# Performance work log

Hardware: AMD Instinct MI355X
Metric: run time of the kernel (lower is better)

The kernel has to match this reference:

```python
import jax, jax.numpy as jnp
import numpy as np

B, N, D, H, K = 8, 1024, 1024, 64, 20


def setup_inputs() -> dict:
    key = jax.random.key(0)
    ks = jax.random.split(key, 8)
    s = 0.05
    return {
        "f1": jax.random.normal(ks[0], (B, N, D), jnp.float32),
        "f2": jax.random.normal(ks[1], (B, N, D), jnp.float32),
        "W1a": jax.random.normal(ks[2], (D, H), jnp.float32) * s,
        "b1a": jnp.zeros((H,), jnp.float32),
        "W2a": jax.random.normal(ks[3], (H, H), jnp.float32) * s,
        "b2a": jnp.zeros((H,), jnp.float32),
        "W1b": jax.random.normal(ks[4], (H, H), jnp.float32) * s,
        "b1b": jnp.zeros((H,), jnp.float32),
        "W2b": jax.random.normal(ks[5], (H, H), jnp.float32) * s,
        "b2b": jnp.zeros((H,), jnp.float32),
        "k": K,
    }


def _knn_idx(f, k):
    # f: [N, D] -> indices [N, k] of k nearest neighbors (self excluded)
    sq = jnp.sum(f * f, axis=-1)                      # [N]
    d = sq[:, None] + sq[None, :] - 2.0 * (f @ f.T)   # [N, N] squared dists
    n = f.shape[0]
    d = d + jnp.eye(n, dtype=f.dtype) * jnp.float32(1e10)  # exclude self-loop
    _, idx = jax.lax.top_k(-d, k)                     # smallest distances
    return idx


def _gin_layer(x, idx, W1, b1, W2, b2):
    # GINConv with eps=0: MLP(x + sum_{j in N(i)} x_j)
    agg = jnp.sum(x[idx], axis=1)                     # [N, D] neighbor-sum
    h = x + agg
    h = jnp.maximum(h @ W1 + b1, 0.0) @ W2 + b2
    return h


def reference(f1, f2, W1a, b1a, W2a, b2a, W1b, b1b, W2b, b2b, k):
    def encode(f):
        idx = _knn_idx(f, k)
        h = _gin_layer(f, idx, W1a, b1a, W2a, b2a)
        h = _gin_layer(h, idx, W1b, b1b, W2b, b2b)
        return h

    def per_sample(a, b):
        z1 = encode(a)                                # [N, H]
        z2 = encode(b)                                # [N, H]
        sim = z1 @ z2.T                               # [N, N]
        return jax.nn.softmax(sim, axis=1)

    return jax.vmap(per_sample)(f1, f2)               # [B, N, N]
```

## Files before the change

kernel.cpp:

```cpp
#include <hip/hip_runtime.h>
#include <hip/hip_bf16.h>
#include <math.h>

#define BATCH 8
#define NPTS  1024
#define DIM   1024
#define HID   64
#define KNN   20
#define NMAT  16
#define KPACK 3072

typedef __attribute__((ext_vector_type(8))) short short8;
typedef __attribute__((ext_vector_type(4))) float floatx4;

__device__ __forceinline__ const float* mat_base(const float* f1, const float* f2, int m) {
    return (m < BATCH) ? (f1 + (size_t)m * NPTS * DIM)
                       : (f2 + (size_t)(m - BATCH) * NPTS * DIM);
}

__device__ __forceinline__ unsigned short f2bf_bits(float v) {
    __hip_bfloat16 h = __float2bfloat16(v);
    return *(unsigned short*)&h;
}
__device__ __forceinline__ float bfbits2f(unsigned short b) {
    union { unsigned u; float f; } c; c.u = ((unsigned)b) << 16; return c.f;
}

__global__ __launch_bounds__(256) void split_ymlp_kernel(const float* __restrict__ f1,
                                                         const float* __restrict__ f2,
                                                         const float* __restrict__ W,
                                                         unsigned short* __restrict__ H,
                                                         float* __restrict__ sq,
                                                         float* __restrict__ y) {
    int row0 = blockIdx.x * 64;
    int m = row0 >> 10;
    const float* A = mat_base(f1, f2, m) + (size_t)(row0 & (NPTS - 1)) * DIM;
    unsigned short* Hb = H + (size_t)row0 * KPACK;
    __shared__ float As[64][20];
    __shared__ float Ws[16][HID];
    int tid = threadIdx.x;
    int r = tid >> 2, cq = (tid & 3) * 4;
    int ty = tid >> 4, tx = tid & 15;
    float acc[4][4];
    #pragma unroll
    for (int i = 0; i < 4; ++i)
        #pragma unroll
        for (int j = 0; j < 4; ++j) acc[i][j] = 0.f;
    float sqp = 0.f;
    unsigned short* Hr = Hb + (size_t)r * KPACK + cq;

    for (int kk = 0; kk < DIM; kk += 16) {
        float4 a = *(const float4*)&A[(size_t)r * DIM + kk + cq];
        {
            float vv[4] = {a.x, a.y, a.z, a.w};
            unsigned short h1[4], h2[4], h3[4];
            #pragma unroll
            for (int c = 0; c < 4; ++c) {
                unsigned short b1 = f2bf_bits(vv[c]);
                float r1 = vv[c] - bfbits2f(b1);
                unsigned short b2 = f2bf_bits(r1);
                float r2 = r1 - bfbits2f(b2);
                unsigned short b3 = f2bf_bits(r2);
                h1[c] = b1; h2[c] = b2; h3[c] = b3;
            }
            *(ushort4*)&Hr[kk]        = *(ushort4*)&h1[0];
            *(ushort4*)&Hr[1024 + kk] = *(ushort4*)&h2[0];
            *(ushort4*)&Hr[2048 + kk] = *(ushort4*)&h3[0];
            sqp += a.x * a.x + a.y * a.y + a.z * a.z + a.w * a.w;
        }
        *(float4*)&As[r][cq] = a;
        {
            int d = tid >> 4, hh = (tid & 15) * 4;
            *(float4*)&Ws[d][hh] = *(const float4*)&W[(size_t)(kk + d) * HID + hh];
        }
        __syncthreads();
        #pragma unroll
        for (int k = 0; k < 16; ++k) {
            float av[4];
            #pragma unroll
            for (int ii = 0; ii < 4; ++ii) av[ii] = As[ty * 4 + ii][k];
            float4 w = *(const float4*)&Ws[k][tx * 4];
            #pragma unroll
            for (int ii = 0; ii < 4; ++ii) {
                acc[ii][0] += av[ii] * w.x;
                acc[ii][1] += av[ii] * w.y;
                acc[ii][2] += av[ii] * w.z;
                acc[ii][3] += av[ii] * w.w;
            }
        }
        __syncthreads();
    }
    sqp += __shfl_down(sqp, 1);
    sqp += __shfl_down(sqp, 2);
    if ((tid & 3) == 0) sq[row0 + r] = sqp;
    #pragma unroll
    for (int ii = 0; ii < 4; ++ii)
        *(float4*)&y[(size_t)(row0 + ty * 4 + ii) * HID + tx * 4] = *(float4*)&acc[ii][0];
}

#define GRAM_STEP(CURAF, NXTAF, CBUF, NBUF, KN, ISSUE, WAITOP)                             \
  {                                                                                        \
    if (ISSUE) {                                                                           \
      _Pragma("unroll")                                                                    \
      for (int s = 0; s < 3; ++s)                                                          \
        _Pragma("unroll")                                                                  \
        for (int a = 0; a < 2; ++a)                                                        \
          NXTAF[s][a] = *(const short8*)&Hm[(size_t)(ti + ((w << 1) + a) * 16 + r16) * KPACK \
                                            + (size_t)(s << 10) + (KN) + (kc << 3)];       \
      _Pragma("unroll")                                                                    \
      for (int c = 0; c < 6; ++c) {                                                        \
        int ca = w * 6 + c; int seg = ca >> 3; int rb = ca & 7;                            \
        const unsigned short* gb = Hm + (size_t)(tj + rb * 16 + r16) * KPACK               \
                                      + (size_t)(seg << 10) + (KN) + (kc << 3);            \
        __builtin_amdgcn_global_load_lds(                                                  \
            (const __attribute__((address_space(1))) void*)gb,                             \
            (__attribute__((address_space(3))) void*)&Bsl[NBUF][ca * 512], 16, 0, 0);      \
      }                                                                                    \
    }                                                                                      \
    asm volatile(WAITOP ::: "memory");                                                     \
    __builtin_amdgcn_s_barrier();                                                          \
    asm volatile("" ::: "memory");                                                         \
    __builtin_amdgcn_s_setprio(1);                                                         \
    _Pragma("unroll")                                                                      \
    for (int sb = 0; sb < 3; ++sb) {                                                       \
      short8 bf[8];                                                                        \
      _Pragma("unroll")                                                                    \
      for (int b = 0; b < 8; ++b)                                                          \
        bf[b] = *(const short8*)&Bsl[CBUF][(sb * 8 + b) * 512 + lane * 8];                 \
      _Pragma("unroll")                                                                    \
      for (int sa = 0; sa < 3; ++sa) {                                                     \
        if (sa + sb > 2) continue;                                                         \
        _Pragma("unroll")                                                                  \
        for (int a = 0; a < 2; ++a)                                                        \
          _Pragma("unroll")                                                                \
          for (int b = 0; b < 8; ++b)                                                      \
            acc[a][b] = __builtin_amdgcn_mfma_f32_16x16x32_bf16(CURAF[sa][a], bf[b],       \
                                                                acc[a][b], 0, 0, 0);       \
      }                                                                                    \
    }                                                                                      \
    __builtin_amdgcn_s_setprio(0);                                                         \
    asm volatile("" ::: "memory");                                                         \
    __builtin_amdgcn_s_barrier();                                                          \
  }

__global__ __launch_bounds__(256, 2) void gram_mfma_kernel(const unsigned short* __restrict__ H,
                                                           const float* __restrict__ sq,
                                                           float* __restrict__ dist) {
    int bid = blockIdx.x;
    int xcd = bid & 7;
    int g = bid >> 3;
    int m = xcd + 8 * (g & 1);
    int t = g >> 1;
    int bi = 0;
    { int a = t; while (a >= 8 - bi) { a -= 8 - bi; ++bi; } t = a; }
    int bj = bi + t;
    int ti = bi << 7, tj = bj << 7;

    const unsigned short* Hm = H + (size_t)m * NPTS * KPACK;

    __shared__ __align__(16) unsigned short Bsl[3][24 * 512];

    int tid = threadIdx.x;
    int w = tid >> 6, lane = tid & 63;
    int r16 = lane & 15, kc = lane >> 4;

    floatx4 acc[2][8];
    #pragma unroll
    for (int a = 0; a < 2; ++a)
        #pragma unroll
        for (int b = 0; b < 8; ++b) acc[a][b] = (floatx4)0.f;

    short8 afA[3][2], afB[3][2], afC[3][2];

    #pragma unroll
    for (int s = 0; s < 3; ++s)
        #pragma unroll
        for (int a = 0; a < 2; ++a) {
            size_t rowb = (size_t)(ti + ((w << 1) + a) * 16 + r16) * KPACK + (size_t)(s << 10) + (kc << 3);
            afA[s][a] = *(const short8*)&Hm[rowb];
            afB[s][a] = *(const short8*)&Hm[rowb + 32];
        }
    #pragma unroll
    for (int c = 0; c < 6; ++c) {
        int ca = w * 6 + c; int seg = ca >> 3; int rb = ca & 7;
        const unsigned short* gb = Hm + (size_t)(tj + rb * 16 + r16) * KPACK
                                      + (size_t)(seg << 10) + (kc << 3);
        __builtin_amdgcn_global_load_lds(
            (const __attribute__((address_space(1))) void*)gb,
            (__attribute__((address_space(3))) void*)&Bsl[0][ca * 512], 16, 0, 0);
        __builtin_amdgcn_global_load_lds(
            (const __attribute__((address_space(1))) void*)(gb + 32),
            (__attribute__((address_space(3))) void*)&Bsl[1][ca * 512], 16, 0, 0);
    }

    #pragma unroll 1
    for (int t2 = 0; t2 < 30; t2 += 3) {
        GRAM_STEP(afA, afC, 0, 2, (t2 + 2) * 32, 1, "s_waitcnt vmcnt(24)");
        GRAM_STEP(afB, afA, 1, 0, (t2 + 3) * 32, 1, "s_waitcnt vmcnt(24)");
        GRAM_STEP(afC, afB, 2, 1, (t2 + 4) * 32, 1, "s_waitcnt vmcnt(24)");
    }
    GRAM_STEP(afA, afC, 0, 2, 0, 0, "s_waitcnt vmcnt(12)");
    GRAM_STEP(afB, afC, 1, 2, 0, 0, "s_waitcnt vmcnt(0)");

    const float* sqm = sq + m * NPTS;
    #pragma unroll
    for (int a = 0; a < 2; ++a) {
        int i0 = ti + ((w << 1) + a) * 16 + (lane >> 4) * 4;
        #pragma unroll
        for (int b = 0; b < 8; ++b) {
            int j = tj + b * 16 + (lane & 15);
            float sqj = sqm[j];
            #pragma unroll
            for (int r = 0; r < 4; ++r) {
                int i = i0 + r;
                float v = sqm[i] + sqj - 2.f * acc[a][b][r];
                if (i == j) v += 1e10f;
                dist[((size_t)m * NPTS + i) * NPTS + j] = v;
                if (bi != bj) dist[((size_t)m * NPTS + j) * NPTS + i] = v;
            }
        }
    }
}

__global__ __launch_bounds__(256) void topk_kernel(const float* __restrict__ dist,
                                                   int* __restrict__ knn_idx) {
    int tid = threadIdx.x;
    int wave = tid >> 6, lane = tid & 63;
    int row = blockIdx.x * 4 + wave;
    const float* d = dist + (size_t)row * NPTS;
    float v[16];
    #pragma unroll
    for (int s = 0; s < 16; ++s) v[s] = d[s * 64 + lane];
    int myj = 0;
    for (int sel = 0; sel < KNN; ++sel) {
        float bv = v[0]; int bs = 0;
        #pragma unroll
        for (int s = 1; s < 16; ++s)
            if (v[s] < bv) { bv = v[s]; bs = s; }
        int bj = bs * 64 + lane;
        #pragma unroll
        for (int off = 1; off < 64; off <<= 1) {
            float ov = __shfl_xor(bv, off);
            int   oj = __shfl_xor(bj, off);
            if (ov < bv || (ov == bv && oj < bj)) { bv = ov; bj = oj; }
        }
        if ((bj & 63) == lane) v[bj >> 6] = 3e38f;
        if (lane == sel) myj = bj;
    }
    if (lane < KNN) knn_idx[(size_t)row * KNN + lane] = myj;
}

__global__ __launch_bounds__(256) void t1h1_kernel(const float* __restrict__ y,
                                                   const int* __restrict__ knn_idx,
                                                   const float* __restrict__ W,
                                                   const float* __restrict__ bias1,
                                                   const float* __restrict__ bias2,
                                                   float* __restrict__ h1) {
    int row0 = blockIdx.x * 64;
    int m = row0 >> 10;
    __shared__ int nb[64 * KNN];
    __shared__ float t1s[64][65];
    __shared__ float Ws[64][HID];
    __shared__ float b1s[HID], b2s[HID];
    int tid = threadIdx.x;
    for (int k = tid; k < 64 * KNN; k += 256) nb[k] = knn_idx[(size_t)row0 * KNN + k];
    for (int k = tid; k < 64 * HID; k += 256) Ws[k >> 6][k & 63] = W[k];
    if (tid < HID) { b1s[tid] = bias1[tid]; b2s[tid] = bias2[tid]; }
    __syncthreads();
    {
        int r = tid >> 2, c0 = (tid & 3) * 16;
        const float* yr = y + (size_t)(row0 + r) * HID + c0;
        float4 a[4];
        #pragma unroll
        for (int q = 0; q < 4; ++q) a[q] = *(const float4*)&yr[q * 4];
        const float* ym = y + (size_t)(m << 10) * HID;
        #pragma unroll
        for (int t = 0; t < KNN; ++t) {
            const float* yn = ym + (size_t)nb[r * KNN + t] * HID + c0;
            #pragma unroll
            for (int q = 0; q < 4; ++q) {
                float4 v = *(const float4*)&yn[q * 4];
                a[q].x += v.x; a[q].y += v.y; a[q].z += v.z; a[q].w += v.w;
            }
        }
        #pragma unroll
        for (int q = 0; q < 4; ++q) {
            int c = c0 + q * 4;
            t1s[r][c + 0] = fmaxf(a[q].x + b1s[c + 0], 0.f);
            t1s[r][c + 1] = fmaxf(a[q].y + b1s[c + 1], 0.f);
            t1s[r][c + 2] = fmaxf(a[q].z + b1s[c + 2], 0.f);
            t1s[r][c + 3] = fmaxf(a[q].w + b1s[c + 3], 0.f);
        }
    }
    __syncthreads();
    int ty = tid >> 4, tx = tid & 15;
    float acc[4][4];
    #pragma unroll
    for (int i = 0; i < 4; ++i)
        #pragma unroll
        for (int j = 0; j < 4; ++j) acc[i][j] = 0.f;
    #pragma unroll
    for (int k = 0; k < HID; ++k) {
        float a[4];
        #pragma unroll
        for (int ii = 0; ii < 4; ++ii) a[ii] = t1s[ty * 4 + ii][k];
        float4 w = *(const float4*)&Ws[k][tx * 4];
        #pragma unroll
        for (int ii = 0; ii < 4; ++ii) {
            acc[ii][0] += a[ii] * w.x;
            acc[ii][1] += a[ii] * w.y;
            acc[ii][2] += a[ii] * w.z;
            acc[ii][3] += a[ii] * w.w;
        }
    }
    #pragma unroll
    for (int ii = 0; ii < 4; ++ii) {
        float o[4];
        #pragma unroll
        for (int jj = 0; jj < 4; ++jj) o[jj] = acc[ii][jj] + b2s[tx * 4 + jj];
        *(float4*)&h1[(size_t)(row0 + ty * 4 + ii) * HID + tx * 4] = *(float4*)&o[0];
    }
}

__global__ __launch_bounds__(256) void t2z_kernel(const float* __restrict__ h1,
                                                  const int* __restrict__ knn_idx,
                                                  const float* __restrict__ W1,
                                                  const float* __restrict__ bias1,
                                                  const float* __restrict__ W2,
                                                  const float* __restrict__ bias2,
                                                  float* __restrict__ z) {
    int row0 = blockIdx.x * 64;
    int m = row0 >> 10;
    __shared__ int nb[64 * KNN];
    __shared__ float hs[64][65];
    __shared__ float t2s[64][65];
    __shared__ float Ws[64][HID];
    __shared__ float b1s[HID], b2s[HID];
    int tid = threadIdx.x;
    for (int k = tid; k < 64 * KNN; k += 256) nb[k] = knn_idx[(size_t)row0 * KNN + k];
    for (int k = tid; k < 64 * HID; k += 256) Ws[k >> 6][k & 63] = W1[k];
    if (tid < HID) { b1s[tid] = bias1[tid]; b2s[tid] = bias2[tid]; }
    __syncthreads();
    {
        int r = tid >> 2, c0 = (tid & 3) * 16;
        const float* hr = h1 + (size_t)(row0 + r) * HID + c0;
        float4 a[4];
        #pragma unroll
        for (int q = 0; q < 4; ++q) a[q] = *(const float4*)&hr[q * 4];
        const float* hm = h1 + (size_t)(m << 10) * HID;
        #pragma unroll
        for (int t = 0; t < KNN; ++t) {
            const float* hn = hm + (size_t)nb[r * KNN + t] * HID + c0;
            #pragma unroll
            for (int q = 0; q < 4; ++q) {
                float4 v = *(const float4*)&hn[q * 4];
                a[q].x += v.x; a[q].y += v.y; a[q].z += v.z; a[q].w += v.w;
            }
        }
        #pragma unroll
        for (int q = 0; q < 4; ++q) *(float4*)&hs[r][c0 + q * 4] = a[q];
    }
    __syncthreads();
    int ty = tid >> 4, tx = tid & 15;
    float acc[4][4];
    #pragma unroll
    for (int i = 0; i < 4; ++i)
        #pragma unroll
        for (int j = 0; j < 4; ++j) acc[i][j] = 0.f;
    #pragma unroll
    for (int k = 0; k < HID; ++k) {
        float a[4];
        #pragma unroll
        for (int ii = 0; ii < 4; ++ii) a[ii] = hs[ty * 4 + ii][k];
        float4 w = *(const float4*)&Ws[k][tx * 4];
        #pragma unroll
        for (int ii = 0; ii < 4; ++ii) {
            acc[ii][0] += a[ii] * w.x;
            acc[ii][1] += a[ii] * w.y;
            acc[ii][2] += a[ii] * w.z;
            acc[ii][3] += a[ii] * w.w;
        }
    }
    #pragma unroll
    for (int ii = 0; ii < 4; ++ii)
        #pragma unroll
        for (int jj = 0; jj < 4; ++jj)
            t2s[ty * 4 + ii][tx * 4 + jj] = fmaxf(acc[ii][jj] + b1s[tx * 4 + jj], 0.f);
    __syncthreads();
    for (int k = tid; k < 64 * HID; k += 256) Ws[k >> 6][k & 63] = W2[k];
    __syncthreads();
    #pragma unroll
    for (int i = 0; i < 4; ++i)
        #pragma unroll
        for (int j = 0; j < 4; ++j) acc[i][j] = 0.f;
    #pragma unroll
    for (int k = 0; k < HID; ++k) {
        float a[4];
        #pragma unroll
        for (int ii = 0; ii < 4; ++ii) a[ii] = t2s[ty * 4 + ii][k];
        float4 w = *(const float4*)&Ws[k][tx * 4];
        #pragma unroll
        for (int ii = 0; ii < 4; ++ii) {
            acc[ii][0] += a[ii] * w.x;
            acc[ii][1] += a[ii] * w.y;
            acc[ii][2] += a[ii] * w.z;
            acc[ii][3] += a[ii] * w.w;
        }
    }
    #pragma unroll
    for (int ii = 0; ii < 4; ++ii) {
        float o[4];
        #pragma unroll
        for (int jj = 0; jj < 4; ++jj) o[jj] = acc[ii][jj] + b2s[tx * 4 + jj];
        *(float4*)&z[(size_t)(row0 + ty * 4 + ii) * HID + tx * 4] = *(float4*)&o[0];
    }
}

__global__ __launch_bounds__(256) void sim_kernel(const float* __restrict__ z,
                                                  float* __restrict__ logits) {
    int bid = blockIdx.x;
    int b = bid >> 8;
    int tile = bid & 255;
    int ti = (tile >> 4) << 6;
    int tj = (tile & 15) << 6;
    const float* z1 = z + (size_t)b * NPTS * HID;
    const float* z2 = z + (size_t)(BATCH + b) * NPTS * HID;
    __shared__ float Z1[64][68];
    __shared__ float Z2[64][68];
    int tid = threadIdx.x;
    #pragma unroll
    for (int i = 0; i < 4; ++i) {
        int l = tid + i * 256;
        int r = l >> 4, c = (l & 15) * 4;
        *(float4*)&Z1[r][c] = *(const float4*)&z1[(size_t)(ti + r) * HID + c];
        *(float4*)&Z2[r][c] = *(const float4*)&z2[(size_t)(tj + r) * HID + c];
    }
    __syncthreads();
    int ty = tid >> 4, tx = tid & 15;
    float acc[4][4];
    #pragma unroll
    for (int i = 0; i < 4; ++i)
        #pragma unroll
        for (int j = 0; j < 4; ++j) acc[i][j] = 0.f;
    #pragma unroll
    for (int h = 0; h < HID; ++h) {
        float a[4], bb[4];
        #pragma unroll
        for (int ii = 0; ii < 4; ++ii) { a[ii] = Z1[ty * 4 + ii][h]; bb[ii] = Z2[tx * 4 + ii][h]; }
        #pragma unroll
        for (int ii = 0; ii < 4; ++ii)
            #pragma unroll
            for (int jj = 0; jj < 4; ++jj)
                acc[ii][jj] += a[ii] * bb[jj];
    }
    #pragma unroll
    for (int ii = 0; ii < 4; ++ii) {
        float* dst = logits + ((size_t)b * NPTS + ti + ty * 4 + ii) * NPTS + tj + tx * 4;
        *(float4*)&dst[0] = *(float4*)&acc[ii][0];
    }
}

__global__ __launch_bounds__(256) void softmax_kernel(const float* __restrict__ logits,
                                                      float* __restrict__ out) {
    int row = blockIdx.x;
    const float* L = logits + (size_t)row * NPTS;
    __shared__ float buf[NPTS];
    __shared__ float red[8];
    int tid = threadIdx.x;
    int wave = tid >> 6, lane = tid & 63;
    float mx = -3e38f;
    #pragma unroll
    for (int s = 0; s < 4; ++s) {
        float v = L[tid + s * 256];
        buf[tid + s * 256] = v;
        mx = fmaxf(mx, v);
    }
    #pragma unroll
    for (int off = 32; off > 0; off >>= 1) mx = fmaxf(mx, __shfl_down(mx, off));
    if (lane == 0) red[wave] = mx;
    __syncthreads();
    mx = fmaxf(fmaxf(red[0], red[1]), fmaxf(red[2], red[3]));
    float sum = 0.f;
    #pragma unroll
    for (int s = 0; s < 4; ++s) {
        float e = expf(buf[tid + s * 256] - mx);
        buf[tid + s * 256] = e;
        sum += e;
    }
    #pragma unroll
    for (int off = 32; off > 0; off >>= 1) sum += __shfl_down(sum, off);
    if (lane == 0) red[4 + wave] = sum;
    __syncthreads();
    float inv = 1.f / (red[4] + red[5] + red[6] + red[7]);
    #pragma unroll
    for (int s = 0; s < 4; ++s)
        out[(size_t)row * NPTS + tid + s * 256] = buf[tid + s * 256] * inv;
}

extern "C" void kernel_launch(void* const* d_in, const int* in_sizes, int n_in,
                              void* d_out, int out_size, void* d_ws, size_t ws_size,
                              hipStream_t stream) {
    const float* f1  = (const float*)d_in[0];
    const float* f2  = (const float*)d_in[1];
    const float* W1a = (const float*)d_in[2];
    const float* b1a = (const float*)d_in[3];
    const float* W2a = (const float*)d_in[4];
    const float* b2a = (const float*)d_in[5];
    const float* W1b = (const float*)d_in[6];
    const float* b1b = (const float*)d_in[7];
    const float* W2b = (const float*)d_in[8];
    const float* b2b = (const float*)d_in[9];
    float* out = (float*)d_out;

    char* ws = (char*)d_ws;
    unsigned short* H = (unsigned short*)ws;
    float* dist = (float*)(ws + (size_t)NMAT * NPTS * KPACK * sizeof(unsigned short));
    float* sq   = dist + (size_t)NMAT * NPTS * NPTS;
    int*   kidx = (int*)(sq + NMAT * NPTS);
    float* ybuf = (float*)(kidx + NMAT * NPTS * KNN);
    float* h1b  = ybuf + (size_t)NMAT * NPTS * HID;
    float* zb   = h1b + (size_t)NMAT * NPTS * HID;

    split_ymlp_kernel<<<NMAT * NPTS / 64, 256, 0, stream>>>(f1, f2, W1a, H, sq, ybuf);
    gram_mfma_kernel<<<NMAT * 36, 256, 0, stream>>>(H, sq, dist);
    topk_kernel<<<NMAT * NPTS / 4, 256, 0, stream>>>(dist, kidx);
    t1h1_kernel<<<NMAT * NPTS / 64, 256, 0, stream>>>(ybuf, kidx, W2a, b1a, b2a, h1b);
    t2z_kernel<<<NMAT * NPTS / 64, 256, 0, stream>>>(h1b, kidx, W1b, b1b, W2b, b2b, zb);
    sim_kernel<<<BATCH * 256, 256, 0, stream>>>(zb, dist);
    softmax_kernel<<<BATCH * NPTS, 256, 0, stream>>>(dist, out);
}
```

Baseline: 523.3 us.

## Enlarge gram kernel tiles to 256x256 with 512-thread blocks

```diff
diff --git a/kernel.cpp b/kernel.cpp
--- a/kernel.cpp
+++ b/kernel.cpp
@@ -98,20 +98,24 @@
         *(float4*)&y[(size_t)(row0 + ty * 4 + ii) * HID + tx * 4] = *(float4*)&acc[ii][0];
 }
 
-#define GRAM_STEP(CURAF, NXTAF, CBUF, NBUF, KN, ISSUE, WAITOP)                             \
+#define GRAM_STEP(CURAF, NXTAF, CBUF, NBUF, T, ISSA, ISSB, WAITOP)                         \
   {                                                                                        \
-    if (ISSUE) {                                                                           \
+    if (ISSA) {                                                                            \
+      int kna = ((T) + 1) * 32;                                                            \
       _Pragma("unroll")                                                                    \
       for (int s = 0; s < 3; ++s)                                                          \
         _Pragma("unroll")                                                                  \
         for (int a = 0; a < 2; ++a)                                                        \
           NXTAF[s][a] = *(const short8*)&Hm[(size_t)(ti + ((w << 1) + a) * 16 + r16) * KPACK \
-                                            + (size_t)(s << 10) + (KN) + (kc << 3)];       \
+                                            + (size_t)(s << 10) + kna + (kc << 3)];        \
+    }                                                                                      \
+    if (ISSB) {                                                                            \
+      int knb = ((T) + 2) * 32;                                                            \
       _Pragma("unroll")                                                                    \
       for (int c = 0; c < 6; ++c) {                                                        \
-        int ca = w * 6 + c; int seg = ca >> 3; int rb = ca & 7;                            \
-        const unsigned short* gb = Hm + (size_t)(tj + rb * 16 + r16) * KPACK               \
-                                      + (size_t)(seg << 10) + (KN) + (kc << 3);            \
+        int ca = w * 6 + c; int seg = ca >> 4; int cbk = ca & 15;                          \
+        const unsigned short* gb = Hm + (size_t)(tj + cbk * 16 + r16) * KPACK              \
+                                      + (size_t)(seg << 10) + knb + (kc << 3);             \
         __builtin_amdgcn_global_load_lds(                                                  \
             (const __attribute__((address_space(1))) void*)gb,                             \
             (__attribute__((address_space(3))) void*)&Bsl[NBUF][ca * 512], 16, 0, 0);      \
@@ -123,19 +127,17 @@
     __builtin_amdgcn_s_setprio(1);                                                         \
     _Pragma("unroll")                                                                      \
     for (int sb = 0; sb < 3; ++sb) {                                                       \
-      short8 bf[8];                                                                        \
       _Pragma("unroll")                                                                    \
-      for (int b = 0; b < 8; ++b)                                                          \
-        bf[b] = *(const short8*)&Bsl[CBUF][(sb * 8 + b) * 512 + lane * 8];                 \
-      _Pragma("unroll")                                                                    \
-      for (int sa = 0; sa < 3; ++sa) {                                                     \
-        if (sa + sb > 2) continue;                                                         \
+      for (int cb = 0; cb < 16; ++cb) {                                                    \
+        short8 bf = *(const short8*)&Bsl[CBUF][(sb * 16 + cb) * 512 + lane * 8];           \
         _Pragma("unroll")                                                                  \
-        for (int a = 0; a < 2; ++a)                                                        \
+        for (int sa = 0; sa < 3; ++sa) {                                                   \
+          if (sa + sb > 2) continue;                                                       \
           _Pragma("unroll")                                                                \
-          for (int b = 0; b < 8; ++b)                                                      \
-            acc[a][b] = __builtin_amdgcn_mfma_f32_16x16x32_bf16(CURAF[sa][a], bf[b],       \
-                                                                acc[a][b], 0, 0, 0);       \
+          for (int a = 0; a < 2; ++a)                                                      \
+            acc[a][cb] = __builtin_amdgcn_mfma_f32_16x16x32_bf16(CURAF[sa][a], bf,         \
+                                                                 acc[a][cb], 0, 0, 0);     \
+        }                                                                                  \
       }                                                                                    \
     }                                                                                      \
     __builtin_amdgcn_s_setprio(0);                                                         \
@@ -143,7 +145,7 @@
     __builtin_amdgcn_s_barrier();                                                          \
   }
 
-__global__ __launch_bounds__(256, 2) void gram_mfma_kernel(const unsigned short* __restrict__ H,
+__global__ __launch_bounds__(512, 2) void gram_mfma_kernel(const unsigned short* __restrict__ H,
                                                            const float* __restrict__ sq,
                                                            float* __restrict__ dist) {
     int bid = blockIdx.x;
@@ -152,68 +154,75 @@
     int m = xcd + 8 * (g & 1);
     int t = g >> 1;
     int bi = 0;
-    { int a = t; while (a >= 8 - bi) { a -= 8 - bi; ++bi; } t = a; }
+    { int a2 = t; while (a2 >= 4 - bi) { a2 -= 4 - bi; ++bi; } t = a2; }
     int bj = bi + t;
-    int ti = bi << 7, tj = bj << 7;
+    int ti = bi << 8, tj = bj << 8;
 
     const unsigned short* Hm = H + (size_t)m * NPTS * KPACK;
 
-    __shared__ __align__(16) unsigned short Bsl[3][24 * 512];
+    __shared__ __align__(16) unsigned short Bsl[3][48 * 512];
 
     int tid = threadIdx.x;
     int w = tid >> 6, lane = tid & 63;
     int r16 = lane & 15, kc = lane >> 4;
 
-    floatx4 acc[2][8];
+    floatx4 acc[2][16];
     #pragma unroll
     for (int a = 0; a < 2; ++a)
         #pragma unroll
-        for (int b = 0; b < 8; ++b) acc[a][b] = (floatx4)0.f;
-
-    short8 afA[3][2], afB[3][2], afC[3][2];
+        for (int b = 0; b < 16; ++b) acc[a][b] = (floatx4)0.f;
+
+    short8 afA[3][2], afB[3][2];
 
     #pragma unroll
     for (int s = 0; s < 3; ++s)
         #pragma unroll
-        for (int a = 0; a < 2; ++a) {
-            size_t rowb = (size_t)(ti + ((w << 1) + a) * 16 + r16) * KPACK + (size_t)(s << 10) + (kc << 3);
-            afA[s][a] = *(const short8*)&Hm[rowb];
-            afB[s][a] = *(const short8*)&Hm[rowb + 32];
-        }
+        for (int a = 0; a < 2; ++a)
+            afA[s][a] = *(const short8*)&Hm[(size_t)(ti + ((w << 1) + a) * 16 + r16) * KPACK
+                                            + (size_t)(s << 10) + (kc << 3)];
     #pragma unroll
     for (int c = 0; c < 6; ++c) {
-        int ca = w * 6 + c; int seg = ca >> 3; int rb = ca & 7;
-        const unsigned short* gb = Hm + (size_t)(tj + rb * 16 + r16) * KPACK
+        int ca = w * 6 + c; int seg = ca >> 4; int cbk = ca & 15;
+        const unsigned short* gb = Hm + (size_t)(tj + cbk * 16 + r16) * KPACK
                                       + (size_t)(seg << 10) + (kc << 3);
         __builtin_amdgcn_global_load_lds(
             (const __attribute__((address_space(1))) void*)gb,
             (__attribute__((address_space(3))) void*)&Bsl[0][ca * 512], 16, 0, 0);
+    }
+    #pragma unroll
+    for (int c = 0; c < 6; ++c) {
+        int ca = w * 6 + c; int seg = ca >> 4; int cbk = ca & 15;
+        const unsigned short* gb = Hm + (size_t)(tj + cbk * 16 + r16) * KPACK
+                                      + (size_t)(seg << 10) + 32 + (kc << 3);
         __builtin_amdgcn_global_load_lds(
-            (const __attribute__((address_space(1))) void*)(gb + 32),
+            (const __attribute__((address_space(1))) void*)gb,
             (__attribute__((address_space(3))) void*)&Bsl[1][ca * 512], 16, 0, 0);
     }
 
     #pragma unroll 1
-    for (int t2 = 0; t2 < 30; t2 += 3) {
-        GRAM_STEP(afA, afC, 0, 2, (t2 + 2) * 32, 1, "s_waitcnt vmcnt(24)");
-        GRAM_STEP(afB, afA, 1, 0, (t2 + 3) * 32, 1, "s_waitcnt vmcnt(24)");
-        GRAM_STEP(afC, afB, 2, 1, (t2 + 4) * 32, 1, "s_waitcnt vmcnt(24)");
-    }
-    GRAM_STEP(afA, afC, 0, 2, 0, 0, "s_waitcnt vmcnt(12)");
-    GRAM_STEP(afB, afC, 1, 2, 0, 0, "s_waitcnt vmcnt(0)");
+    for (int t6 = 0; t6 < 30; t6 += 6) {
+        GRAM_STEP(afA, afB, 0, 2, t6 + 0, 1, 1, "s_waitcnt vmcnt(18)");
+        GRAM_STEP(afB, afA, 1, 0, t6 + 1, 1, 1, "s_waitcnt vmcnt(18)");
+        GRAM_STEP(afA, afB, 2, 1, t6 + 2, 1, 1, "s_waitcnt vmcnt(18)");
+        GRAM_STEP(afB, afA, 0, 2, t6 + 3, 1, 1, "s_waitcnt vmcnt(18)");
+        GRAM_STEP(afA, afB, 1, 0, t6 + 4, 1, 1, "s_waitcnt vmcnt(18)");
+        GRAM_STEP(afB, afA, 2, 1, t6 + 5, 1, 1, "s_waitcnt vmcnt(18)");
+    }
+    GRAM_STEP(afA, afB, 0, 2, 30, 1, 0, "s_waitcnt vmcnt(12)");
+    GRAM_STEP(afB, afA, 1, 0, 31, 0, 0, "s_waitcnt vmcnt(0)");
 
     const float* sqm = sq + m * NPTS;
     #pragma unroll
     for (int a = 0; a < 2; ++a) {
         int i0 = ti + ((w << 1) + a) * 16 + (lane >> 4) * 4;
         #pragma unroll
-        for (int b = 0; b < 8; ++b) {
-            int j = tj + b * 16 + (lane & 15);
+        for (int cb = 0; cb < 16; ++cb) {
+            int j = tj + cb * 16 + (lane & 15);
             float sqj = sqm[j];
             #pragma unroll
             for (int r = 0; r < 4; ++r) {
                 int i = i0 + r;
-                float v = sqm[i] + sqj - 2.f * acc[a][b][r];
+                float v = sqm[i] + sqj - 2.f * acc[a][cb][r];
                 if (i == j) v += 1e10f;
                 dist[((size_t)m * NPTS + i) * NPTS + j] = v;
                 if (bi != bj) dist[((size_t)m * NPTS + j) * NPTS + i] = v;
@@ -522,7 +531,7 @@
     float* zb   = h1b + (size_t)NMAT * NPTS * HID;
 
     split_ymlp_kernel<<<NMAT * NPTS / 64, 256, 0, stream>>>(f1, f2, W1a, H, sq, ybuf);
-    gram_mfma_kernel<<<NMAT * 36, 256, 0, stream>>>(H, sq, dist);
+    gram_mfma_kernel<<<NMAT * 10, 512, 0, stream>>>(H, sq, dist);
     topk_kernel<<<NMAT * NPTS / 4, 256, 0, stream>>>(dist, kidx);
     t1h1_kernel<<<NMAT * NPTS / 64, 256, 0, stream>>>(ybuf, kidx, W2a, b1a, b2a, h1b);
     t2z_kernel<<<NMAT * NPTS / 64, 256, 0, stream>>>(h1b, kidx, W1b, b1b, W2b, b2b, zb);
```

After: 583.8 us. 1.12x slower.

## Compute full gram matrix per tile instead of mirroring symmetric tiles

Applied to the files above, without the earlier changes.

```diff
diff --git a/kernel.cpp b/kernel.cpp
--- a/kernel.cpp
+++ b/kernel.cpp
@@ -97,6 +97,50 @@
     for (int ii = 0; ii < 4; ++ii)
         *(float4*)&y[(size_t)(row0 + ty * 4 + ii) * HID + tx * 4] = *(float4*)&acc[ii][0];
 }
+
+#define GRAM_MFMA_SET(AF_S, BF)                                                            \
+    _Pragma("unroll")                                                                      \
+    for (int a = 0; a < 2; ++a)                                                            \
+      _Pragma("unroll")                                                                    \
+      for (int b = 0; b < 8; ++b)                                                          \
+        acc[a][b] = __builtin_amdgcn_mfma_f32_16x16x32_bf16(AF_S[a], BF[b],                \
+                                                            acc[a][b], 0, 0, 0);
+
+#define GRAM_COMPUTE(CURAF, CBUF)                                                          \
+    if (!lower) {                                                                          \
+      _Pragma("unroll")                                                                    \
+      for (int sb = 0; sb < 3; ++sb) {                                                     \
+        short8 bf[8];                                                                      \
+        _Pragma("unroll")                                                                  \
+        for (int b = 0; b < 8; ++b)                                                        \
+          bf[b] = *(const short8*)&Bsl[CBUF][(sb * 8 + b) * 512 + lane * 8];               \
+        _Pragma("unroll")                                                                  \
+        for (int sa = 0; sa < 3; ++sa) {                                                   \
+          if (sa + sb > 2) continue;                                                       \
+          GRAM_MFMA_SET(CURAF[sa], bf)                                                     \
+        }                                                                                  \
+      }                                                                                    \
+    } else {                                                                               \
+      short8 bfK[8], bfT[8];                                                               \
+      _Pragma("unroll")                                                                    \
+      for (int b = 0; b < 8; ++b)                                                          \
+        bfK[b] = *(const short8*)&Bsl[CBUF][(0 * 8 + b) * 512 + lane * 8];                 \
+      GRAM_MFMA_SET(CURAF[0], bfK)                                              \
+      _Pragma("unroll")                                                                    \
+      for (int b = 0; b < 8; ++b)                                                          \
+        bfT[b] = *(const short8*)&Bsl[CBUF][(1 * 8 + b) * 512 + lane * 8];                 \
+      GRAM_MFMA_SET(CURAF[0], bfT)                                              \
+      _Pragma("unroll")                                                                    \
+      for (int b = 0; b < 8; ++b)                                                          \
+        bfT[b] = *(const short8*)&Bsl[CBUF][(2 * 8 + b) * 512 + lane * 8];                 \
+      GRAM_MFMA_SET(CURAF[0], bfT)                                              \
+      GRAM_MFMA_SET(CURAF[1], bfK)                                              \
+      _Pragma("unroll")                                                                    \
+      for (int b = 0; b < 8; ++b)                                                          \
+        bfT[b] = *(const short8*)&Bsl[CBUF][(1 * 8 + b) * 512 + lane * 8];                 \
+      GRAM_MFMA_SET(CURAF[1], bfT)                                              \
+      GRAM_MFMA_SET(CURAF[2], bfK)                                              \
+    }
 
 #define GRAM_STEP(CURAF, NXTAF, CBUF, NBUF, KN, ISSUE, WAITOP)                             \
   {                                                                                        \
@@ -121,23 +165,7 @@
     __builtin_amdgcn_s_barrier();                                                          \
     asm volatile("" ::: "memory");                                                         \
     __builtin_amdgcn_s_setprio(1);                                                         \
-    _Pragma("unroll")                                                                      \
-    for (int sb = 0; sb < 3; ++sb) {                                                       \
-      short8 bf[8];                                                                        \
-      _Pragma("unroll")                                                                    \
-      for (int b = 0; b < 8; ++b)                                                          \
-        bf[b] = *(const short8*)&Bsl[CBUF][(sb * 8 + b) * 512 + lane * 8];                 \
-      _Pragma("unroll")                                                                    \
-      for (int sa = 0; sa < 3; ++sa) {                                                     \
-        if (sa + sb > 2) continue;                                                         \
-        _Pragma("unroll")                                                                  \
-        for (int a = 0; a < 2; ++a)                                                        \
-          _Pragma("unroll")                                                                \
-          for (int b = 0; b < 8; ++b)                                                      \
-            acc[a][b] = __builtin_amdgcn_mfma_f32_16x16x32_bf16(CURAF[sa][a], bf[b],       \
-                                                                acc[a][b], 0, 0, 0);       \
-      }                                                                                    \
-    }                                                                                      \
+    GRAM_COMPUTE(CURAF, CBUF)                                                              \
     __builtin_amdgcn_s_setprio(0);                                                         \
     asm volatile("" ::: "memory");                                                         \
     __builtin_amdgcn_s_barrier();                                                          \
@@ -149,14 +177,9 @@
     int bid = blockIdx.x;
     int xcd = bid & 7;
     int g = bid >> 3;
-    int m = xcd + 8 * (g & 1);
-    int t = g >> 1;
-    int bi = 0;
-    { int a = t; while (a >= 8 - bi) { a -= 8 - bi; ++bi; } t = a; }
-    int bj = bi + t;
+    int bi = g >> 3, bj = g & 7;
     int ti = bi << 7, tj = bj << 7;
-
-    const unsigned short* Hm = H + (size_t)m * NPTS * KPACK;
+    bool lower = bi > bj;
 
     __shared__ __align__(16) unsigned short Bsl[3][24 * 512];
 
@@ -164,59 +187,65 @@
     int w = tid >> 6, lane = tid & 63;
     int r16 = lane & 15, kc = lane >> 4;
 
-    floatx4 acc[2][8];
-    #pragma unroll
-    for (int a = 0; a < 2; ++a)
-        #pragma unroll
-        for (int b = 0; b < 8; ++b) acc[a][b] = (floatx4)0.f;
-
-    short8 afA[3][2], afB[3][2], afC[3][2];
-
-    #pragma unroll
-    for (int s = 0; s < 3; ++s)
+    #pragma unroll 1
+    for (int job = 0; job < 2; ++job) {
+        int m = xcd + 8 * job;
+        const unsigned short* Hm = H + (size_t)m * NPTS * KPACK;
+
+        floatx4 acc[2][8];
+        #pragma unroll
+        for (int a = 0; a < 2; ++a)
+            #pragma unroll
+            for (int b = 0; b < 8; ++b) acc[a][b] = (floatx4)0.f;
+
+        short8 afA[3][2], afB[3][2], afC[3][2];
+
+        #pragma unroll
+        for (int s = 0; s < 3; ++s)
+            #pragma unroll
+            for (int a = 0; a < 2; ++a) {
+                size_t rowb = (size_t)(ti + ((w << 1) + a) * 16 + r16) * KPACK
+                              + (size_t)(s << 10) + (kc << 3);
+                afA[s][a] = *(const short8*)&Hm[rowb];
+                afB[s][a] = *(const short8*)&Hm[rowb + 32];
+            }
+        #pragma unroll
+        for (int c = 0; c < 6; ++c) {
+            int ca = w * 6 + c; int seg = ca >> 3; int rb = ca & 7;
+            const unsigned short* gb = Hm + (size_t)(tj + rb * 16 + r16) * KPACK
+                                          + (size_t)(seg << 10) + (kc << 3);
+            __builtin_amdgcn_global_load_lds(
+                (const __attribute__((address_space(1))) void*)gb,
+                (__attribute__((address_space(3))) void*)&Bsl[0][ca * 512], 16, 0, 0);
+            __builtin_amdgcn_global_load_lds(
+                (const __attribute__((address_space(1))) void*)(gb + 32),
+                (__attribute__((address_space(3))) void*)&Bsl[1][ca * 512], 16, 0, 0);
+        }
+
+        #pragma unroll 1
+        for (int t2 = 0; t2 < 30; t2 += 3) {
+            GRAM_STEP(afA, afC, 0, 2, (t2 + 2) * 32, 1, "s_waitcnt vmcnt(24)");
+            GRAM_STEP(afB, afA, 1, 0, (t2 + 3) * 32, 1, "s_waitcnt vmcnt(24)");
+            GRAM_STEP(afC, afB, 2, 1, (t2 + 4) * 32, 1, "s_waitcnt vmcnt(24)");
+        }
+        GRAM_STEP(afA, afC, 0, 2, 0, 0, "s_waitcnt vmcnt(12)");
+        GRAM_STEP(afB, afC, 1, 2, 0, 0, "s_waitcnt vmcnt(0)");
+
+        const float* sqm = sq + m * NPTS;
         #pragma unroll
         for (int a = 0; a < 2; ++a) {
-            size_t rowb = (size_t)(ti + ((w << 1) + a) * 16 + r16) * KPACK + (size_t)(s << 10) + (kc << 3);
-            afA[s][a] = *(const short8*)&Hm[rowb];
-            afB[s][a] = *(const short8*)&Hm[rowb + 32];
-        }
-    #pragma unroll
-    for (int c = 0; c < 6; ++c) {
-        int ca = w * 6 + c; int seg = ca >> 3; int rb = ca & 7;
-        const unsigned short* gb = Hm + (size_t)(tj + rb * 16 + r16) * KPACK
-                                      + (size_t)(seg << 10) + (kc << 3);
-        __builtin_amdgcn_global_load_lds(
-            (const __attribute__((address_space(1))) void*)gb,
-            (__attribute__((address_space(3))) void*)&Bsl[0][ca * 512], 16, 0, 0);
-        __builtin_amdgcn_global_load_lds(
-            (const __attribute__((address_space(1))) void*)(gb + 32),
-            (__attribute__((address_space(3))) void*)&Bsl[1][ca * 512], 16, 0, 0);
-    }
-
-    #pragma unroll 1
-    for (int t2 = 0; t2 < 30; t2 += 3) {
-        GRAM_STEP(afA, afC, 0, 2, (t2 + 2) * 32, 1, "s_waitcnt vmcnt(24)");
-        GRAM_STEP(afB, afA, 1, 0, (t2 + 3) * 32, 1, "s_waitcnt vmcnt(24)");
-        GRAM_STEP(afC, afB, 2, 1, (t2 + 4) * 32, 1, "s_waitcnt vmcnt(24)");
-    }
-    GRAM_STEP(afA, afC, 0, 2, 0, 0, "s_waitcnt vmcnt(12)");
-    GRAM_STEP(afB, afC, 1, 2, 0, 0, "s_waitcnt vmcnt(0)");
-
-    const float* sqm = sq + m * NPTS;
-    #pragma unroll
-    for (int a = 0; a < 2; ++a) {
-        int i0 = ti + ((w << 1) + a) * 16 + (lane >> 4) * 4;
-        #pragma unroll
-        for (int b = 0; b < 8; ++b) {
-            int j = tj + b * 16 + (lane & 15);
-            float sqj = sqm[j];
-            #pragma unroll
-            for (int r = 0; r < 4; ++r) {
-                int i = i0 + r;
-                float v = sqm[i] + sqj - 2.f * acc[a][b][r];
-                if (i == j) v += 1e10f;
-                dist[((size_t)m * NPTS + i) * NPTS + j] = v;
-                if (bi != bj) dist[((size_t)m * NPTS + j) * NPTS + i] = v;
+            int i0 = ti + ((w << 1) + a) * 16 + (lane >> 4) * 4;
+            #pragma unroll
+            for (int b = 0; b < 8; ++b) {
+                int j = tj + b * 16 + (lane & 15);
+                float sqj = sqm[j];
+                #pragma unroll
+                for (int r = 0; r < 4; ++r) {
+                    int i = i0 + r;
+                    float v = sqm[i] + sqj - 2.f * acc[a][b][r];
+                    if (i == j) v += 1e10f;
+                    dist[((size_t)m * NPTS + i) * NPTS + j] = v;
+                }
             }
         }
     }
@@ -522,7 +551,7 @@
     float* zb   = h1b + (size_t)NMAT * NPTS * HID;
 
     split_ymlp_kernel<<<NMAT * NPTS / 64, 256, 0, stream>>>(f1, f2, W1a, H, sq, ybuf);
-    gram_mfma_kernel<<<NMAT * 36, 256, 0, stream>>>(H, sq, dist);
+    gram_mfma_kernel<<<512, 256, 0, stream>>>(H, sq, dist);
     topk_kernel<<<NMAT * NPTS / 4, 256, 0, stream>>>(dist, kidx);
     t1h1_kernel<<<NMAT * NPTS / 64, 256, 0, stream>>>(ybuf, kidx, W2a, b1a, b2a, h1b);
     t2z_kernel<<<NMAT * NPTS / 64, 256, 0, stream>>>(h1b, kidx, W1b, b1b, W2b, b2b, zb);
```

After: 772.4 us. +47.6%, slower.

## Fuse similarity GEMM and row softmax into one kernel

Applied to the files above, without the earlier changes.

```diff
diff --git a/kernel.cpp b/kernel.cpp
--- a/kernel.cpp
+++ b/kernel.cpp
@@ -416,85 +416,81 @@
     }
 }
 
-__global__ __launch_bounds__(256) void sim_kernel(const float* __restrict__ z,
-                                                  float* __restrict__ logits) {
+__global__ __launch_bounds__(256) void simsoftmax_kernel(const float* __restrict__ z,
+                                                         float* __restrict__ out) {
     int bid = blockIdx.x;
-    int b = bid >> 8;
-    int tile = bid & 255;
-    int ti = (tile >> 4) << 6;
-    int tj = (tile & 15) << 6;
-    const float* z1 = z + (size_t)b * NPTS * HID;
+    int b = bid >> 5;
+    int r0 = (bid & 31) * 32;
+    const float* z1 = z + (size_t)b * NPTS * HID + (size_t)r0 * HID;
     const float* z2 = z + (size_t)(BATCH + b) * NPTS * HID;
-    __shared__ float Z1[64][68];
+    __shared__ float S[32][1024];
     __shared__ float Z2[64][68];
+    __shared__ float Z1[32][64];
     int tid = threadIdx.x;
-    #pragma unroll
-    for (int i = 0; i < 4; ++i) {
-        int l = tid + i * 256;
-        int r = l >> 4, c = (l & 15) * 4;
-        *(float4*)&Z1[r][c] = *(const float4*)&z1[(size_t)(ti + r) * HID + c];
-        *(float4*)&Z2[r][c] = *(const float4*)&z2[(size_t)(tj + r) * HID + c];
-    }
-    __syncthreads();
+    {
+        int r = tid >> 3, c = (tid & 7) * 8;
+        *(float4*)&Z1[r][c]     = *(const float4*)&z1[(size_t)r * HID + c];
+        *(float4*)&Z1[r][c + 4] = *(const float4*)&z1[(size_t)r * HID + c + 4];
+    }
     int ty = tid >> 4, tx = tid & 15;
-    float acc[4][4];
-    #pragma unroll
-    for (int i = 0; i < 4; ++i)
-        #pragma unroll
-        for (int j = 0; j < 4; ++j) acc[i][j] = 0.f;
-    #pragma unroll
-    for (int h = 0; h < HID; ++h) {
-        float a[4], bb[4];
-        #pragma unroll
-        for (int ii = 0; ii < 4; ++ii) { a[ii] = Z1[ty * 4 + ii][h]; bb[ii] = Z2[tx * 4 + ii][h]; }
-        #pragma unroll
-        for (int ii = 0; ii < 4; ++ii)
-            #pragma unroll
-            for (int jj = 0; jj < 4; ++jj)
-                acc[ii][jj] += a[ii] * bb[jj];
-    }
-    #pragma unroll
-    for (int ii = 0; ii < 4; ++ii) {
-        float* dst = logits + ((size_t)b * NPTS + ti + ty * 4 + ii) * NPTS + tj + tx * 4;
-        *(float4*)&dst[0] = *(float4*)&acc[ii][0];
-    }
-}
-
-__global__ __launch_bounds__(256) void softmax_kernel(const float* __restrict__ logits,
-                                                      float* __restrict__ out) {
-    int row = blockIdx.x;
-    const float* L = logits + (size_t)row * NPTS;
-    __shared__ float buf[NPTS];
-    __shared__ float red[8];
-    int tid = threadIdx.x;
-    int wave = tid >> 6, lane = tid & 63;
-    float mx = -3e38f;
-    #pragma unroll
-    for (int s = 0; s < 4; ++s) {
-        float v = L[tid + s * 256];
-        buf[tid + s * 256] = v;
-        mx = fmaxf(mx, v);
-    }
-    #pragma unroll
-    for (int off = 32; off > 0; off >>= 1) mx = fmaxf(mx, __shfl_down(mx, off));
-    if (lane == 0) red[wave] = mx;
-    __syncthreads();
-    mx = fmaxf(fmaxf(red[0], red[1]), fmaxf(red[2], red[3]));
-    float sum = 0.f;
-    #pragma unroll
-    for (int s = 0; s < 4; ++s) {
-        float e = expf(buf[tid + s * 256] - mx);
-        buf[tid + s * 256] = e;
-        sum += e;
-    }
-    #pragma unroll
-    for (int off = 32; off > 0; off >>= 1) sum += __shfl_down(sum, off);
-    if (lane == 0) red[4 + wave] = sum;
-    __syncthreads();
-    float inv = 1.f / (red[4] + red[5] + red[6] + red[7]);
-    #pragma unroll
-    for (int s = 0; s < 4; ++s)
-        out[(size_t)row * NPTS + tid + s * 256] = buf[tid + s * 256] * inv;
+    for (int jt = 0; jt < 16; ++jt) {
+        __syncthreads();
+        {
+            int r = tid >> 2, c = (tid & 3) * 16;
+            const float* zr = z2 + (size_t)(jt * 64 + r) * HID + c;
+            *(float4*)&Z2[r][c]      = *(const float4*)&zr[0];
+            *(float4*)&Z2[r][c + 4]  = *(const float4*)&zr[4];
+            *(float4*)&Z2[r][c + 8]  = *(const float4*)&zr[8];
+            *(float4*)&Z2[r][c + 12] = *(const float4*)&zr[12];
+        }
+        __syncthreads();
+        float acc[2][4];
+        #pragma unroll
+        for (int i = 0; i < 2; ++i)
+            #pragma unroll
+            for (int j = 0; j < 4; ++j) acc[i][j] = 0.f;
+        #pragma unroll
+        for (int h = 0; h < HID; ++h) {
+            float a[2], bb[4];
+            #pragma unroll
+            for (int i = 0; i < 2; ++i) a[i] = Z1[ty * 2 + i][h];
+            #pragma unroll
+            for (int j = 0; j < 4; ++j) bb[j] = Z2[tx * 4 + j][h];
+            #pragma unroll
+            for (int i = 0; i < 2; ++i)
+                #pragma unroll
+                for (int j = 0; j < 4; ++j)
+                    acc[i][j] += a[i] * bb[j];
+        }
+        #pragma unroll
+        for (int i = 0; i < 2; ++i)
+            *(float4*)&S[ty * 2 + i][jt * 64 + tx * 4] = *(float4*)&acc[i][0];
+    }
+    __syncthreads();
+    int wv = tid >> 6, lane = tid & 63;
+    #pragma unroll 1
+    for (int rr = 0; rr < 8; ++rr) {
+        int r = wv * 8 + rr;
+        float mx = -3e38f;
+        #pragma unroll
+        for (int s = 0; s < 16; ++s) mx = fmaxf(mx, S[r][lane + s * 64]);
+        #pragma unroll
+        for (int off = 32; off > 0; off >>= 1) mx = fmaxf(mx, __shfl_xor(mx, off));
+        float sum = 0.f;
+        #pragma unroll
+        for (int s = 0; s < 16; ++s) {
+            float e = expf(S[r][lane + s * 64] - mx);
+            S[r][lane + s * 64] = e;
+            sum += e;
+        }
+        #pragma unroll
+        for (int off = 32; off > 0; off >>= 1) sum += __shfl_xor(sum, off);
+        float inv = 1.f / sum;
+        float* orow = out + ((size_t)b * NPTS + r0 + r) * NPTS;
+        #pragma unroll
+        for (int s = 0; s < 16; ++s)
+            orow[lane + s * 64] = S[r][lane + s * 64] * inv;
+    }
 }
 
 extern "C" void kernel_launch(void* const* d_in, const int* in_sizes, int n_in,
@@ -526,6 +522,5 @@
     topk_kernel<<<NMAT * NPTS / 4, 256, 0, stream>>>(dist, kidx);
     t1h1_kernel<<<NMAT * NPTS / 64, 256, 0, stream>>>(ybuf, kidx, W2a, b1a, b2a, h1b);
     t2z_kernel<<<NMAT * NPTS / 64, 256, 0, stream>>>(h1b, kidx, W1b, b1b, W2b, b2b, zb);
-    sim_kernel<<<BATCH * 256, 256, 0, stream>>>(zb, dist);
-    softmax_kernel<<<BATCH * NPTS, 256, 0, stream>>>(dist, out);
-}
+    simsoftmax_kernel<<<BATCH * 32, 256, 0, stream>>>(zb, out);
+}
```

Result: slower. 565.6 us (+8.1%).
